# Performance work log

Measured on AMD Instinct MI355X. Metric: run time of the kernel, lower is better.

## Reference

```python
import jax, jax.numpy as jnp
import numpy as np

B, N, C_IN, C_OUT = 2, 512, 64, 64  # mid_dim == out_dim
EPS = 1e-5

def _bn(x, g, b):
    # PyTorch BatchNorm1d in training mode: biased batch stats over axis 0 of [M, C]
    mu = x.mean(axis=0)
    var = x.var(axis=0)
    return (x - mu) * jax.lax.rsqrt(var + EPS) * g + b

def setup_inputs() -> dict:
    key = jax.random.key(0)
    ks = jax.random.split(key, 16)
    s = 0.05
    return {
        "pos": jax.random.normal(ks[0], (B, N, 3), jnp.float32),
        "c_features": jax.random.normal(ks[1], (B, N, C_IN), jnp.float32),
        "Wq": jax.random.normal(ks[2], (C_OUT, C_IN), jnp.float32) * s,
        "bq": jnp.zeros((C_OUT,), jnp.float32),
        "Wk": jax.random.normal(ks[3], (C_OUT, C_IN), jnp.float32) * s,
        "bk": jnp.zeros((C_OUT,), jnp.float32),
        "Wv": jax.random.normal(ks[4], (C_OUT, C_IN), jnp.float32) * s,
        "bv": jnp.zeros((C_OUT,), jnp.float32),
        "Wp1": jax.random.normal(ks[5], (3, 3), jnp.float32) * s,
        "bp1": jnp.zeros((3,), jnp.float32),
        "g_p": jnp.ones((3,), jnp.float32),
        "b_p": jnp.zeros((3,), jnp.float32),
        "Wp2": jax.random.normal(ks[6], (C_OUT, 3), jnp.float32) * s,
        "bp2": jnp.zeros((C_OUT,), jnp.float32),
        "g_w": jnp.ones((C_OUT,), jnp.float32),
        "b_w": jnp.zeros((C_OUT,), jnp.float32),
        "Ww1": jax.random.normal(ks[7], (C_OUT, C_OUT), jnp.float32) * s,
        "bw1": jnp.zeros((C_OUT,), jnp.float32),
        "Ww2": jax.random.normal(ks[8], (C_OUT, C_OUT), jnp.float32) * s,
        "bw2": jnp.zeros((C_OUT,), jnp.float32),
    }

def reference(pos, c_features, Wq, bq, Wk, bk, Wv, bv, Wp1, bp1, g_p, b_p, Wp2, bp2, g_w, b_w, Ww1, bw1, Ww2, bw2):
    b, n = pos.shape[0], pos.shape[1]
    q = c_features @ Wq.T + bq                       # [B,N,Cmid]
    k = c_features @ Wk.T + bk
    v = c_features @ Wv.T + bv                       # [B,N,Cout]
    rel = pos[:, :, None, :] - pos[:, None, :, :]    # [B,N,N,3]
    h = rel.reshape(-1, 3) @ Wp1.T + bp1             # [B*N*N,3]
    h = jax.nn.relu(_bn(h, g_p, b_p))
    delta = (h @ Wp2.T + bp2).reshape(b, n, n, -1)   # [B,N,N,Cmid]
    qk = q[:, :, None, :] - k[:, None, :, :] + delta # [B,N,N,Cmid]
    h2 = _bn(qk.reshape(-1, qk.shape[-1]), g_w, b_w)
    h2 = jax.nn.relu(h2)
    h2 = jax.nn.relu(h2 @ Ww1.T + bw1)
    w = (h2 @ Ww2.T + bw2).reshape(b, n, n, -1)      # [B,N,N,Cout]
    attn = jax.nn.softmax(w, axis=2)                 # softmax over j
    out = jnp.sum(attn * (v[:, None, :, :] + delta), axis=2)  # [B,N,Cout]
    return out
```

## Files before the change

kernel.cpp:

```cpp
#include <hip/hip_runtime.h>
#include <stdint.h>
#include <stddef.h>

#define DEV __device__ __forceinline__

typedef __attribute__((ext_vector_type(4))) float f32x4;
typedef __attribute__((ext_vector_type(8))) short bf16x8;

union FragU { bf16x8 f; uint32_t u[4]; };

DEV uint32_t pk_bf16(float a, float b) {
  uint32_t d;
  asm("v_cvt_pk_bf16_f32 %0, %1, %2" : "=v"(d) : "v"(a), "v"(b));
  return d;
}

DEV uint16_t f2bf(float x) {
  uint32_t u = __float_as_uint(x);
  u += 0x7fffu + ((u >> 16) & 1u);
  return (uint16_t)(u >> 16);
}

__launch_bounds__(256)
__global__ void kAll(const float* __restrict__ cf, const float* __restrict__ pos,
                     const float* __restrict__ Wq, const float* __restrict__ Wk,
                     const float* __restrict__ Wv, const float* __restrict__ bq,
                     const float* __restrict__ bk, const float* __restrict__ bv,
                     const float* __restrict__ Ww1, const float* __restrict__ Ww2,
                     const float* __restrict__ Wp1, const float* __restrict__ g_p,
                     const float* __restrict__ b_p, const float* __restrict__ bp2,
                     float* __restrict__ qo, float* __restrict__ ko,
                     float* __restrict__ vT, uint16_t* __restrict__ W1bf,
                     uint16_t* __restrict__ W2bf, float* __restrict__ hpa,
                     float* __restrict__ Mpart, float* __restrict__ XPp,
                     float* __restrict__ SNp) {
  const int bid = blockIdx.x, t = threadIdx.x;

  __shared__ __align__(16) float Ush[4160];
  __shared__ __align__(16) f32x4 X[512];
  __shared__ float redr[64][4][4];
  __shared__ float mred[256][6];
  __shared__ float mred2[64][6];
  __shared__ float rfin[64][4];
  __shared__ float redn[256][2];
  __shared__ float wred[4][2][9];
  __shared__ float a1L[3];

  if (bid < 128) {
    const int c = t & 63, rr = t >> 6;
    const int r0 = bid * 8;
    float accq[2], acck[2], accv[2];
    for (int m = 0; m < 3; ++m) {
      __syncthreads();
      const float* Wm = (m == 0) ? Wq : ((m == 1) ? Wk : Wv);
      for (int idx = t; idx < 4096; idx += 256)
        Ush[(idx & 63) * 65 + (idx >> 6)] = Wm[idx];
      __syncthreads();
#pragma unroll
      for (int rp = 0; rp < 2; ++rp) {
        const int row = r0 + rr + 4 * rp;
        const float* cfr = cf + (size_t)row * 64;
        float a = 0.f;
#pragma unroll 8
        for (int kk = 0; kk < 64; ++kk)
          a = fmaf(cfr[kk], Ush[kk * 65 + c], a);
        if (m == 0) accq[rp] = a;
        else if (m == 1) acck[rp] = a;
        else accv[rp] = a;
      }
    }
#pragma unroll
    for (int rp = 0; rp < 2; ++rp) {
      const int bn = r0 + rr + 4 * rp;
      qo[(size_t)bn * 64 + c] = accq[rp] + bq[c];
      ko[(size_t)bn * 64 + c] = acck[rp] + bk[c];
    }
    float* vb = (float*)X;
    const float bvv = bv[c] + bp2[c];
    vb[c * 12 + rr] = accv[0] + bvv;
    vb[c * 12 + rr + 4] = accv[1] + bvv;
    __syncthreads();
    if (t < 128) {
      const int c2 = t >> 1, hf = t & 1;
      const f32x4 v = *(const f32x4*)(vb + c2 * 12 + 4 * hf);
      *(f32x4*)(vT + ((size_t)(r0 >> 9) * 64 + c2) * 512 + (r0 & 511) + 4 * hf) = v;
    }
  } else if (bid == 128) {
    const float L2E = 1.4426950408889634f;
    for (int idx = t; idx < 8192; idx += 256) {
      const int m = idx >> 12;
      const int r = idx & 4095;
      const int f = r >> 9;
      const int l = (r >> 3) & 63;
      const int e = r & 7;
      const int nt = f >> 1, ks = f & 1, lm = l & 15, lq = l >> 4;
      const int row = 16 * nt + lm, col = 8 * lq + 32 * ks + e;
      const float src = m ? (Ww2[row * 64 + col] * L2E) : Ww1[row * 64 + col];
      (m ? W2bf : W1bf)[r] = f2bf(src);
    }
  } else {
    const int sb = bid - 129;
    const int s = sb >> 4, b = (sb >> 3) & 1, chunk = sb & 7;
    const int r0g = b * 512 + chunk * 64;

    {
      const int w = t >> 6, c = t & 63;
      const float* wr = (s ? Wk : Wq) + c * 64;
      const float bias = s ? bk[c] : (bq[c] + bp2[c]);
      f32x4 wreg[16];
#pragma unroll
      for (int kv = 0; kv < 16; ++kv) wreg[kv] = *(const f32x4*)(wr + kv * 4);
      for (int m = 0; m < 16; ++m) {
        const int row = w * 16 + m;
        const f32x4* cfr = (const f32x4*)(cf + (size_t)(r0g + row) * 64);
        float a0 = bias, a1v = 0.f, a2v = 0.f, a3v = 0.f;
#pragma unroll
        for (int kv = 0; kv < 16; ++kv) {
          const f32x4 f = cfr[kv];
          a0 = fmaf(f.x, wreg[kv].x, a0);
          a1v = fmaf(f.y, wreg[kv].y, a1v);
          a2v = fmaf(f.z, wreg[kv].z, a2v);
          a3v = fmaf(f.w, wreg[kv].w, a3v);
        }
        Ush[row * 64 + c] = (a0 + a1v) + (a2v + a3v);
      }
    }

    {
      const int l = t & 63, wid = t >> 6;
      for (int b2 = 0; b2 < 2; ++b2) {
        float s9[9] = {0, 0, 0, 0, 0, 0, 0, 0, 0};
        for (int r = 0; r < 2; ++r) {
          const int row = t + 256 * r;
          const float* p = pos + (size_t)(b2 * 512 + row) * 3;
          const float p0 = p[0], p1 = p[1], p2 = p[2];
          s9[0] += p0; s9[1] += p1; s9[2] += p2;
          s9[3] += p0 * p0; s9[4] += p0 * p1; s9[5] += p0 * p2;
          s9[6] += p1 * p1; s9[7] += p1 * p2; s9[8] += p2 * p2;
        }
#pragma unroll
        for (int a = 0; a < 9; ++a) {
          float v = s9[a];
          v += __shfl_xor(v, 1);  v += __shfl_xor(v, 2);  v += __shfl_xor(v, 4);
          v += __shfl_xor(v, 8);  v += __shfl_xor(v, 16); v += __shfl_xor(v, 32);
          s9[a] = v;
        }
        if (l == 0) {
#pragma unroll
          for (int a = 0; a < 9; ++a) wred[wid][b2][a] = s9[a];
        }
      }
    }
    __syncthreads();
    if (t == 0) {
      float C[6] = {0, 0, 0, 0, 0, 0};
      const float invM = 1.0f / 524288.0f;
      for (int b2 = 0; b2 < 2; ++b2) {
        float acc9[9];
#pragma unroll
        for (int a = 0; a < 9; ++a)
          acc9[a] = wred[0][b2][a] + wred[1][b2][a] + wred[2][b2][a] + wred[3][b2][a];
        C[0] += 1024.f * acc9[3] - 2.f * acc9[0] * acc9[0];
        C[1] += 1024.f * acc9[4] - 2.f * acc9[0] * acc9[1];
        C[2] += 1024.f * acc9[5] - 2.f * acc9[0] * acc9[2];
        C[3] += 1024.f * acc9[6] - 2.f * acc9[1] * acc9[1];
        C[4] += 1024.f * acc9[7] - 2.f * acc9[1] * acc9[2];
        C[5] += 1024.f * acc9[8] - 2.f * acc9[2] * acc9[2];
      }
      for (int a = 0; a < 6; ++a) C[a] *= invM;
      for (int tt = 0; tt < 3; ++tt) {
        const float w0 = Wp1[tt * 3 + 0], w1 = Wp1[tt * 3 + 1], w2 = Wp1[tt * 3 + 2];
        const float var = w0 * w0 * C[0] + w1 * w1 * C[3] + w2 * w2 * C[5]
                        + 2.f * (w0 * w1 * C[1] + w0 * w2 * C[2] + w1 * w2 * C[4]);
        a1L[tt] = g_p[tt] * rsqrtf(var + 1e-5f);
      }
    }
    __syncthreads();

    {
      const float a10 = a1L[0], a11 = a1L[1], a12 = a1L[2];
      const float w00 = Wp1[0], w01 = Wp1[1], w02 = Wp1[2];
      const float w10 = Wp1[3], w11 = Wp1[4], w12 = Wp1[5];
      const float w20 = Wp1[6], w21 = Wp1[7], w22 = Wp1[8];
      for (int r = 0; r < 2; ++r) {
        const int row = t + 256 * r;
        const float* p = pos + (size_t)(b * 512 + row) * 3;
        const float p0 = p[0], p1 = p[1], p2 = p[2];
        f32x4 v;
        v.x = a10 * (w00 * p0 + w01 * p1 + w02 * p2);
        v.y = a11 * (w10 * p0 + w11 * p1 + w12 * p2);
        v.z = a12 * (w20 * p0 + w21 * p1 + w22 * p2);
        v.w = 0.f;
        if (s == 0 && chunk == 0)
          *(f32x4*)(hpa + (size_t)(b * 512 + row) * 4) = v;
        if (s) { v.x = -v.x; v.y = -v.y; v.z = -v.z; }
        X[row] = v;
      }
    }
    __syncthreads();

    {
      const int al = t >> 2, qr = t & 3;
      const int a = chunk * 64 + al;
      const f32x4 xa = X[a];
      const float base0 = xa.x + b_p[0], base1 = xa.y + b_p[1], base2 = xa.z + b_p[2];
      float r0 = 0, r1 = 0, r2 = 0;
      float m00 = 0, m01 = 0, m02 = 0, m11 = 0, m12 = 0, m22 = 0;
#pragma unroll 8
      for (int jj = qr * 128; jj < qr * 128 + 128; ++jj) {
        const f32x4 xj = X[jj];
        const float h0 = fmaxf(0.f, base0 - xj.x);
        const float h1 = fmaxf(0.f, base1 - xj.y);
        const float h2 = fmaxf(0.f, base2 - xj.z);
        r0 += h0; r1 += h1; r2 += h2;
        if (s == 0) {
          m00 = fmaf(h0, h0, m00); m01 = fmaf(h0, h1, m01); m02 = fmaf(h0, h2, m02);
          m11 = fmaf(h1, h1, m11); m12 = fmaf(h1, h2, m12); m22 = fmaf(h2, h2, m22);
        }
      }
      redr[al][qr][0] = r0; redr[al][qr][1] = r1; redr[al][qr][2] = r2; redr[al][qr][3] = 0.f;
      mred[t][0] = m00; mred[t][1] = m01; mred[t][2] = m02;
      mred[t][3] = m11; mred[t][4] = m12; mred[t][5] = m22;
    }
    __syncthreads();

    if (t < 64) {
      float sx = 0, sy = 0, sz = 0;
#pragma unroll
      for (int p = 0; p < 4; ++p) { sx += redr[t][p][0]; sy += redr[t][p][1]; sz += redr[t][p][2]; }
      rfin[t][0] = sx; rfin[t][1] = sy; rfin[t][2] = sz; rfin[t][3] = 0.f;
      if (s == 0) {
#pragma unroll
        for (int cc = 0; cc < 6; ++cc)
          mred2[t][cc] = mred[t][cc] + mred[t + 64][cc] + mred[t + 128][cc] + mred[t + 192][cc];
      }
    }
    __syncthreads();

    if (s == 0 && t < 6) {
      float m = 0.f;
      for (int p = 0; p < 64; ++p) m += mred2[p][t];
      Mpart[sb * 12 + t] = m;
    }
    if (s == 0 && t >= 64 && t < 67) {
      const int tt = t - 64;
      float v = 0.f;
#pragma unroll 8
      for (int a = 0; a < 64; ++a) v += rfin[a][tt];
      Mpart[sb * 12 + 6 + tt] = v;
    }
    if (t < 192) {
      const int c = t & 63, tt = t >> 6;
      float xp = 0.f;
#pragma unroll 8
      for (int a = 0; a < 64; ++a) xp = fmaf(Ush[a * 64 + c], rfin[a][tt], xp);
      if (s) xp = -xp;
      XPp[((size_t)sb * 3 + tt) * 64 + c] = xp;
    }
    {
      const int c = t & 63, g = t >> 6;
      float su = 0.f, su2 = 0.f;
#pragma unroll
      for (int r = 0; r < 16; ++r) {
        const float v = Ush[(g * 16 + r) * 64 + c];
        su += v;
        su2 = fmaf(v, v, su2);
      }
      redn[t][0] = su; redn[t][1] = su2;
    }
    __syncthreads();
    if (t < 64) {
      float a0 = 0.f, a1v = 0.f;
#pragma unroll
      for (int p = 0; p < 4; ++p) { a0 += redn[t + 64 * p][0]; a1v += redn[t + 64 * p][1]; }
      SNp[((size_t)sb * 2 + 0) * 64 + t] = a0;
      SNp[((size_t)sb * 2 + 1) * 64 + t] = a1v;
    }
  }
}

__launch_bounds__(256)
__global__ void k3_main(const float* __restrict__ q, const float* __restrict__ kk_,
                        const float* __restrict__ vT, const float* __restrict__ hpa,
                        const float* __restrict__ Mpart, const float* __restrict__ XPp,
                        const float* __restrict__ SNp, const float* __restrict__ g_w,
                        const float* __restrict__ b_w,
                        const uint16_t* __restrict__ W1bf, const uint16_t* __restrict__ W2bf,
                        const float* __restrict__ bp2, const float* __restrict__ Wp2,
                        const float* __restrict__ b_p, const float* __restrict__ bw1g,
                        const float* __restrict__ bw2g, float* __restrict__ out) {
  const int bid = blockIdx.x;
  const int b = bid >> 9, i = bid & 511;
  const int t = threadIdx.x;
  const int wid = t >> 6, l = t & 63;
  const int lm = l & 15, lq = l >> 4;

  __shared__ __align__(16) uint16_t W1l[4096];
  __shared__ __align__(16) uint16_t W2l[4096];
  __shared__ __align__(16) uint16_t H2[4][16][76];
  __shared__ __align__(16) float P0[64];
  __shared__ __align__(16) float a2s[64];
  __shared__ __align__(16) float Pts[3][64];
  __shared__ __align__(16) float comb[4][64][2];
  __shared__ float xps[4][3][64];
  __shared__ float sns[4][2][64];
  __shared__ float msh[12];

  {
    *(bf16x8*)(&W1l[t * 16])     = *(const bf16x8*)(W1bf + t * 16);
    *(bf16x8*)(&W1l[t * 16 + 8]) = *(const bf16x8*)(W1bf + t * 16 + 8);
    *(bf16x8*)(&W2l[t * 16])     = *(const bf16x8*)(W2bf + t * 16);
    *(bf16x8*)(&W2l[t * 16 + 8]) = *(const bf16x8*)(W2bf + t * 16 + 8);
  }

  {
    const int qd = t >> 6, c = t & 63;
    float x0 = 0, x1 = 0, x2 = 0, s0 = 0, s1 = 0;
#pragma unroll
    for (int p = 0; p < 8; ++p) {
      const int blk = qd * 8 + p;
      x0 += XPp[((size_t)blk * 3 + 0) * 64 + c];
      x1 += XPp[((size_t)blk * 3 + 1) * 64 + c];
      x2 += XPp[((size_t)blk * 3 + 2) * 64 + c];
      s0 += SNp[((size_t)blk * 2 + 0) * 64 + c];
      s1 += SNp[((size_t)blk * 2 + 1) * 64 + c];
    }
    xps[qd][0][c] = x0; xps[qd][1][c] = x1; xps[qd][2][c] = x2;
    sns[qd][0][c] = s0; sns[qd][1][c] = s1;
    if (t < 12) {
      float m = 0.f;
#pragma unroll
      for (int p = 0; p < 16; ++p) m += Mpart[p * 12 + t];
      msh[t] = m;
    }
  }
  __syncthreads();

  if (t < 64) {
    const int c = t;
    const float URd0 = xps[0][0][c] + xps[1][0][c] + xps[2][0][c] + xps[3][0][c];
    const float URd1 = xps[0][1][c] + xps[1][1][c] + xps[2][1][c] + xps[3][1][c];
    const float URd2 = xps[0][2][c] + xps[1][2][c] + xps[2][2][c] + xps[3][2][c];
    const float Su0 = sns[0][0][c], Su20 = sns[0][1][c];
    const float Su1 = sns[1][0][c], Su21 = sns[1][1][c];
    const float Sk0 = sns[2][0][c], Sk20 = sns[2][1][c];
    const float Sk1 = sns[3][0][c], Sk21 = sns[3][1][c];
    const float P0t = Wp2[c * 3 + 0], P1t = Wp2[c * 3 + 1], P2t = Wp2[c * 3 + 2];
    const float Nf = 512.f, invM = 1.f / 524288.f;
    float S1 = Nf * (Su0 - Sk0) + Nf * (Su1 - Sk1);
    const float Q2 = Nf * Su20 - 2.f * Su0 * Sk0 + Nf * Sk20
                   + Nf * Su21 - 2.f * Su1 * Sk1 + Nf * Sk21;
    const float Xc = P0t * URd0 + P1t * URd1 + P2t * URd2;
    S1 += P0t * msh[6] + P1t * msh[7] + P2t * msh[8];
    const float Hm = P0t * P0t * msh[0] + 2.f * P0t * P1t * msh[1] + 2.f * P0t * P2t * msh[2]
                   + P1t * P1t * msh[3] + 2.f * P1t * P2t * msh[4] + P2t * P2t * msh[5];
    const float E1 = S1 * invM;
    const float E2 = (Q2 + 2.f * Xc + Hm) * invM;
    const float var = E2 - E1 * E1;
    const float A2 = g_w[c] * rsqrtf(var + 1e-5f);
    const float be2 = b_w[c] - E1 * A2;
    a2s[c] = A2;
    P0[c] = fmaf(A2, q[(size_t)(b * 512 + i) * 64 + c] + bp2[c], be2);
    Pts[0][c] = A2 * P0t;
    Pts[1][c] = A2 * P1t;
    Pts[2][c] = A2 * P2t;
  }

  const f32x4 hi = *(const f32x4*)(hpa + (size_t)(b * 512 + i) * 4);
  const float bb0 = b_p[0], bb1 = b_p[1], bb2 = b_p[2];
  const float LOG2E = 1.4426950408889634f;

  float bw1r[4], bw2l[4], wpa[4], wpb[4], wpc[4];
#pragma unroll
  for (int nt = 0; nt < 4; ++nt) {
    const int c = 16 * nt + lm;
    bw1r[nt] = bw1g[c];
    bw2l[nt] = bw2g[c] * LOG2E;
    wpa[nt] = Wp2[c * 3 + 0];
    wpb[nt] = Wp2[c * 3 + 1];
    wpc[nt] = Wp2[c * 3 + 2];
  }

  float l_[4] = {0.f, 0.f, 0.f, 0.f};
  float acc_[4] = {0.f, 0.f, 0.f, 0.f};

  __syncthreads();

  const float* kbase = kk_ + (size_t)(b * 512) * 64;
  const float* hbase = hpa + (size_t)(b * 512) * 4;
  const float* vTb = vT + (size_t)b * 64 * 512;

  f32x4 kvA[2][2];
  {
    const int j0 = wid * 16 + lm;
#pragma unroll
    for (int ks = 0; ks < 2; ++ks) {
      kvA[ks][0] = *(const f32x4*)(kbase + (size_t)j0 * 64 + 32 * ks + 8 * lq);
      kvA[ks][1] = *(const f32x4*)(kbase + (size_t)j0 * 64 + 32 * ks + 8 * lq + 4);
    }
  }

  for (int it = 0; it < 8; ++it) {
    const int jb = it * 64 + wid * 16;
    const int j = jb + lm;
    const int j2 = jb + 4 * lq;

    f32x4 kvN[2][2];
    if (it < 7) {
      const int jn = j + 64;
#pragma unroll
      for (int ks = 0; ks < 2; ++ks) {
        kvN[ks][0] = *(const f32x4*)(kbase + (size_t)jn * 64 + 32 * ks + 8 * lq);
        kvN[ks][1] = *(const f32x4*)(kbase + (size_t)jn * 64 + 32 * ks + 8 * lq + 4);
      }
    }

    const f32x4 hj = *(const f32x4*)(hbase + j * 4);
    f32x4 hjr[4];
#pragma unroll
    for (int r = 0; r < 4; ++r) hjr[r] = *(const f32x4*)(hbase + (j2 + r) * 4);
    f32x4 vv[4];
#pragma unroll
    for (int nt = 0; nt < 4; ++nt)
      vv[nt] = *(const f32x4*)(vTb + (size_t)(16 * nt + lm) * 512 + j2);

    const float h0 = fmaxf(0.f, hi.x - hj.x + bb0);
    const float h1 = fmaxf(0.f, hi.y - hj.y + bb1);
    const float h2v = fmaxf(0.f, hi.z - hj.z + bb2);

    FragU A1[2];
#pragma unroll
    for (int ks = 0; ks < 2; ++ks) {
      const int c0 = 32 * ks + 8 * lq;
      f32x4 pv[2], av[2], t0[2], t1[2], t2[2];
      pv[0] = *(const f32x4*)(P0 + c0);        pv[1] = *(const f32x4*)(P0 + c0 + 4);
      av[0] = *(const f32x4*)(a2s + c0);       av[1] = *(const f32x4*)(a2s + c0 + 4);
      t0[0] = *(const f32x4*)(&Pts[0][c0]);    t0[1] = *(const f32x4*)(&Pts[0][c0 + 4]);
      t1[0] = *(const f32x4*)(&Pts[1][c0]);    t1[1] = *(const f32x4*)(&Pts[1][c0 + 4]);
      t2[0] = *(const f32x4*)(&Pts[2][c0]);    t2[1] = *(const f32x4*)(&Pts[2][c0 + 4]);
      float x[8];
#pragma unroll
      for (int e = 0; e < 8; ++e) {
        const int hh = e >> 2, e4 = e & 3;
        float xv = pv[hh][e4] - av[hh][e4] * kvA[ks][hh][e4];
        xv = fmaf(t0[hh][e4], h0, xv);
        xv = fmaf(t1[hh][e4], h1, xv);
        xv = fmaf(t2[hh][e4], h2v, xv);
        x[e] = fmaxf(0.f, xv);
      }
      A1[ks].u[0] = pk_bf16(x[0], x[1]);
      A1[ks].u[1] = pk_bf16(x[2], x[3]);
      A1[ks].u[2] = pk_bf16(x[4], x[5]);
      A1[ks].u[3] = pk_bf16(x[6], x[7]);
    }

    f32x4 d1[4];
    __builtin_amdgcn_s_setprio(1);
#pragma unroll
    for (int nt = 0; nt < 4; ++nt) {
      FragU b0, b1;
      b0.f = *(const bf16x8*)(&W1l[((nt * 2 + 0) * 64 + l) * 8]);
      b1.f = *(const bf16x8*)(&W1l[((nt * 2 + 1) * 64 + l) * 8]);
      f32x4 z = {bw1r[nt], bw1r[nt], bw1r[nt], bw1r[nt]};
      z = __builtin_amdgcn_mfma_f32_16x16x32_bf16(A1[0].f, b0.f, z, 0, 0, 0);
      z = __builtin_amdgcn_mfma_f32_16x16x32_bf16(A1[1].f, b1.f, z, 0, 0, 0);
      d1[nt] = z;
    }
    __builtin_amdgcn_s_setprio(0);

    uint16_t (*h2w)[76] = H2[wid];
#pragma unroll
    for (int nt = 0; nt < 4; ++nt) {
      const uint32_t u01 = pk_bf16(fmaxf(0.f, d1[nt][0]), fmaxf(0.f, d1[nt][1]));
      const uint32_t u23 = pk_bf16(fmaxf(0.f, d1[nt][2]), fmaxf(0.f, d1[nt][3]));
      const int col = 16 * nt + lm;
      h2w[4 * lq + 0][col] = (uint16_t)(u01 & 0xffffu);
      h2w[4 * lq + 1][col] = (uint16_t)(u01 >> 16);
      h2w[4 * lq + 2][col] = (uint16_t)(u23 & 0xffffu);
      h2w[4 * lq + 3][col] = (uint16_t)(u23 >> 16);
    }

    FragU A2[2];
    A2[0].f = *(const bf16x8*)(&h2w[lm][8 * lq]);
    A2[1].f = *(const bf16x8*)(&h2w[lm][32 + 8 * lq]);

    f32x4 d2[4];
    __builtin_amdgcn_s_setprio(1);
#pragma unroll
    for (int nt = 0; nt < 4; ++nt) {
      FragU b0, b1;
      b0.f = *(const bf16x8*)(&W2l[((nt * 2 + 0) * 64 + l) * 8]);
      b1.f = *(const bf16x8*)(&W2l[((nt * 2 + 1) * 64 + l) * 8]);
      f32x4 z = {bw2l[nt], bw2l[nt], bw2l[nt], bw2l[nt]};
      z = __builtin_amdgcn_mfma_f32_16x16x32_bf16(A2[0].f, b0.f, z, 0, 0, 0);
      z = __builtin_amdgcn_mfma_f32_16x16x32_bf16(A2[1].f, b1.f, z, 0, 0, 0);
      d2[nt] = z;
    }
    __builtin_amdgcn_s_setprio(0);

    float hr0[4], hr1[4], hr2[4];
#pragma unroll
    for (int r = 0; r < 4; ++r) {
      hr0[r] = fmaxf(0.f, hi.x - hjr[r].x + bb0);
      hr1[r] = fmaxf(0.f, hi.y - hjr[r].y + bb1);
      hr2[r] = fmaxf(0.f, hi.z - hjr[r].z + bb2);
    }

#pragma unroll
    for (int nt = 0; nt < 4; ++nt) {
      float p[4], val[4];
#pragma unroll
      for (int r = 0; r < 4; ++r) {
        p[r] = __builtin_amdgcn_exp2f(d2[nt][r]);
        float v0 = vv[nt][r];
        v0 = fmaf(wpa[nt], hr0[r], v0);
        v0 = fmaf(wpb[nt], hr1[r], v0);
        v0 = fmaf(wpc[nt], hr2[r], v0);
        val[r] = v0;
      }
      l_[nt] += (p[0] + p[1]) + (p[2] + p[3]);
      float a = acc_[nt];
      a = fmaf(p[0], val[0], a);
      a = fmaf(p[1], val[1], a);
      a = fmaf(p[2], val[2], a);
      a = fmaf(p[3], val[3], a);
      acc_[nt] = a;
    }

    if (it < 7) {
#pragma unroll
      for (int ks = 0; ks < 2; ++ks) {
        kvA[ks][0] = kvN[ks][0];
        kvA[ks][1] = kvN[ks][1];
      }
    }
  }

#pragma unroll
  for (int nt = 0; nt < 4; ++nt) {
    l_[nt] += __shfl_xor(l_[nt], 16);
    acc_[nt] += __shfl_xor(acc_[nt], 16);
    l_[nt] += __shfl_xor(l_[nt], 32);
    acc_[nt] += __shfl_xor(acc_[nt], 32);
  }
  if (lq == 0) {
#pragma unroll
    for (int nt = 0; nt < 4; ++nt) {
      comb[wid][16 * nt + lm][0] = l_[nt];
      comb[wid][16 * nt + lm][1] = acc_[nt];
    }
  }
  __syncthreads();
  if (t < 64) {
    float L = 0.f, A = 0.f;
#pragma unroll
    for (int w = 0; w < 4; ++w) {
      L += comb[w][t][0];
      A += comb[w][t][1];
    }
    out[(size_t)(b * 512 + i) * 64 + t] = A / L;
  }
}

extern "C" void kernel_launch(void* const* d_in, const int* in_sizes, int n_in,
                              void* d_out, int out_size, void* d_ws, size_t ws_size,
                              hipStream_t stream) {
  (void)in_sizes; (void)n_in; (void)out_size; (void)ws_size;
  const float* pos = (const float*)d_in[0];
  const float* cf  = (const float*)d_in[1];
  const float* Wq  = (const float*)d_in[2];
  const float* bq  = (const float*)d_in[3];
  const float* Wk  = (const float*)d_in[4];
  const float* bk  = (const float*)d_in[5];
  const float* Wv  = (const float*)d_in[6];
  const float* bv  = (const float*)d_in[7];
  const float* Wp1 = (const float*)d_in[8];
  const float* g_p = (const float*)d_in[10];
  const float* b_p = (const float*)d_in[11];
  const float* Wp2 = (const float*)d_in[12];
  const float* bp2 = (const float*)d_in[13];
  const float* g_w = (const float*)d_in[14];
  const float* b_w = (const float*)d_in[15];
  const float* Ww1 = (const float*)d_in[16];
  const float* bw1 = (const float*)d_in[17];
  const float* Ww2 = (const float*)d_in[18];
  const float* bw2 = (const float*)d_in[19];

  char* ws = (char*)d_ws;
  uint16_t* W1bf = (uint16_t*)(ws + 0);
  uint16_t* W2bf = (uint16_t*)(ws + 8192);
  float*    hpaw = (float*)(ws + 16896);
  float*    qw   = (float*)(ws + 33280);
  float*    kw   = (float*)(ws + 295424);
  float*    vTw  = (float*)(ws + 557568);
  float*    Mpw  = (float*)(ws + 821248);
  float*    XPpw = (float*)(ws + 823040);
  float*    SNpw = (float*)(ws + 847872);

  kAll<<<dim3(161), dim3(256), 0, stream>>>(cf, pos, Wq, Wk, Wv, bq, bk, bv,
                                            Ww1, Ww2, Wp1, g_p, b_p, bp2,
                                            qw, kw, vTw, W1bf, W2bf, hpaw,
                                            Mpw, XPpw, SNpw);
  k3_main<<<dim3(1024), dim3(256), 0, stream>>>(qw, kw, vTw, hpaw, Mpw, XPpw, SNpw,
                                                g_w, b_w, W1bf, W2bf, bp2, Wp2, b_p,
                                                bw1, bw2, (float*)d_out);
}
```

Baseline: 69.97 us.

## Switch attention MLP to fp16 with packed half2 prologue math and fp16 keys

Replaces the bf16 MFMA path with f16 MFMAs and converts the weight prepacking to fp16. The per-pair BN/affine/ReLU prologue now runs as packed half2 FMAs on fp16 per-channel constants, instead of scalar fp32 math followed by bf16 packing. Keys are stored in fp16, which halves their global load traffic. The s_setprio hints are dropped. The aim is to cut VALU work and memory traffic in the inner loop, at the cost of reduced precision and range in the prologue arithmetic.

```diff
diff --git a/kernel.cpp b/kernel.cpp
--- a/kernel.cpp
+++ b/kernel.cpp
@@ -1,25 +1,18 @@
 #include <hip/hip_runtime.h>
+#include <hip/hip_fp16.h>
 #include <stdint.h>
 #include <stddef.h>
 
 #define DEV __device__ __forceinline__
 
 typedef __attribute__((ext_vector_type(4))) float f32x4;
-typedef __attribute__((ext_vector_type(8))) short bf16x8;
-
-union FragU { bf16x8 f; uint32_t u[4]; };
-
-DEV uint32_t pk_bf16(float a, float b) {
-  uint32_t d;
-  asm("v_cvt_pk_bf16_f32 %0, %1, %2" : "=v"(d) : "v"(a), "v"(b));
-  return d;
-}
-
-DEV uint16_t f2bf(float x) {
-  uint32_t u = __float_as_uint(x);
-  u += 0x7fffu + ((u >> 16) & 1u);
-  return (uint16_t)(u >> 16);
-}
+typedef __attribute__((ext_vector_type(8))) _Float16 f16x8;
+typedef __attribute__((ext_vector_type(2))) _Float16 h2;
+
+union FragH { f16x8 f; uint32_t u[4]; h2 h[4]; };
+union V4H { f32x4 v; h2 h[4]; };
+
+DEV uint16_t f2h(float x) { return __half_as_ushort(__float2half_rn(x)); }
 
 __launch_bounds__(256)
 __global__ void kAll(const float* __restrict__ cf, const float* __restrict__ pos,
@@ -29,9 +22,9 @@
                      const float* __restrict__ Ww1, const float* __restrict__ Ww2,
                      const float* __restrict__ Wp1, const float* __restrict__ g_p,
                      const float* __restrict__ b_p, const float* __restrict__ bp2,
-                     float* __restrict__ qo, float* __restrict__ ko,
-                     float* __restrict__ vT, uint16_t* __restrict__ W1bf,
-                     uint16_t* __restrict__ W2bf, float* __restrict__ hpa,
+                     float* __restrict__ qo, uint16_t* __restrict__ kh,
+                     float* __restrict__ vT, uint16_t* __restrict__ W1h,
+                     uint16_t* __restrict__ W2h, float* __restrict__ hpa,
                      float* __restrict__ Mpart, float* __restrict__ XPp,
                      float* __restrict__ SNp) {
   const int bid = blockIdx.x, t = threadIdx.x;
@@ -73,7 +66,7 @@
     for (int rp = 0; rp < 2; ++rp) {
       const int bn = r0 + rr + 4 * rp;
       qo[(size_t)bn * 64 + c] = accq[rp] + bq[c];
-      ko[(size_t)bn * 64 + c] = acck[rp] + bk[c];
+      kh[(size_t)bn * 64 + c] = f2h(acck[rp] + bk[c]);
     }
     float* vb = (float*)X;
     const float bvv = bv[c] + bp2[c];
@@ -96,7 +89,7 @@
       const int nt = f >> 1, ks = f & 1, lm = l & 15, lq = l >> 4;
       const int row = 16 * nt + lm, col = 8 * lq + 32 * ks + e;
       const float src = m ? (Ww2[row * 64 + col] * L2E) : Ww1[row * 64 + col];
-      (m ? W2bf : W1bf)[r] = f2bf(src);
+      (m ? W2h : W1h)[r] = f2h(src);
     }
   } else {
     const int sb = bid - 129;
@@ -211,11 +204,11 @@
         const f32x4 xj = X[jj];
         const float h0 = fmaxf(0.f, base0 - xj.x);
         const float h1 = fmaxf(0.f, base1 - xj.y);
-        const float h2 = fmaxf(0.f, base2 - xj.z);
-        r0 += h0; r1 += h1; r2 += h2;
+        const float h2v = fmaxf(0.f, base2 - xj.z);
+        r0 += h0; r1 += h1; r2 += h2v;
         if (s == 0) {
-          m00 = fmaf(h0, h0, m00); m01 = fmaf(h0, h1, m01); m02 = fmaf(h0, h2, m02);
-          m11 = fmaf(h1, h1, m11); m12 = fmaf(h1, h2, m12); m22 = fmaf(h2, h2, m22);
+          m00 = fmaf(h0, h0, m00); m01 = fmaf(h0, h1, m01); m02 = fmaf(h0, h2v, m02);
+          m11 = fmaf(h1, h1, m11); m12 = fmaf(h1, h2v, m12); m22 = fmaf(h2v, h2v, m22);
         }
       }
       redr[al][qr][0] = r0; redr[al][qr][1] = r1; redr[al][qr][2] = r2; redr[al][qr][3] = 0.f;
@@ -280,7 +273,7 @@
 }
 
 __launch_bounds__(256)
-__global__ void k3_main(const float* __restrict__ q, const float* __restrict__ kk_,
+__global__ void k3_main(const float* __restrict__ q, const uint16_t* __restrict__ kh,
                         const float* __restrict__ vT, const float* __restrict__ hpa,
                         const float* __restrict__ Mpart, const float* __restrict__ XPp,
                         const float* __restrict__ SNp, const float* __restrict__ g_w,
@@ -298,19 +291,21 @@
   __shared__ __align__(16) uint16_t W1l[4096];
   __shared__ __align__(16) uint16_t W2l[4096];
   __shared__ __align__(16) uint16_t H2[4][16][76];
-  __shared__ __align__(16) float P0[64];
-  __shared__ __align__(16) float a2s[64];
-  __shared__ __align__(16) float Pts[3][64];
+  __shared__ __align__(16) uint16_t P0h[64];
+  __shared__ __align__(16) uint16_t nA2h[64];
+  __shared__ __align__(16) uint16_t Pt0h[64];
+  __shared__ __align__(16) uint16_t Pt1h[64];
+  __shared__ __align__(16) uint16_t Pt2h[64];
   __shared__ __align__(16) float comb[4][64][2];
   __shared__ float xps[4][3][64];
   __shared__ float sns[4][2][64];
   __shared__ float msh[12];
 
   {
-    *(bf16x8*)(&W1l[t * 16])     = *(const bf16x8*)(W1bf + t * 16);
-    *(bf16x8*)(&W1l[t * 16 + 8]) = *(const bf16x8*)(W1bf + t * 16 + 8);
-    *(bf16x8*)(&W2l[t * 16])     = *(const bf16x8*)(W2bf + t * 16);
-    *(bf16x8*)(&W2l[t * 16 + 8]) = *(const bf16x8*)(W2bf + t * 16 + 8);
+    *(f16x8*)(&W1l[t * 16])     = *(const f16x8*)(W1bf + t * 16);
+    *(f16x8*)(&W1l[t * 16 + 8]) = *(const f16x8*)(W1bf + t * 16 + 8);
+    *(f16x8*)(&W2l[t * 16])     = *(const f16x8*)(W2bf + t * 16);
+    *(f16x8*)(&W2l[t * 16 + 8]) = *(const f16x8*)(W2bf + t * 16 + 8);
   }
 
   {
@@ -359,11 +354,11 @@
     const float var = E2 - E1 * E1;
     const float A2 = g_w[c] * rsqrtf(var + 1e-5f);
     const float be2 = b_w[c] - E1 * A2;
-    a2s[c] = A2;
-    P0[c] = fmaf(A2, q[(size_t)(b * 512 + i) * 64 + c] + bp2[c], be2);
-    Pts[0][c] = A2 * P0t;
-    Pts[1][c] = A2 * P1t;
-    Pts[2][c] = A2 * P2t;
+    P0h[c] = f2h(fmaf(A2, q[(size_t)(b * 512 + i) * 64 + c] + bp2[c], be2));
+    nA2h[c] = f2h(-A2);
+    Pt0h[c] = f2h(A2 * P0t);
+    Pt1h[c] = f2h(A2 * P1t);
+    Pt2h[c] = f2h(A2 * P2t);
   }
 
   const f32x4 hi = *(const f32x4*)(hpa + (size_t)(b * 512 + i) * 4);
@@ -386,18 +381,16 @@
 
   __syncthreads();
 
-  const float* kbase = kk_ + (size_t)(b * 512) * 64;
+  const uint16_t* kbase = kh + (size_t)(b * 512) * 64;
   const float* hbase = hpa + (size_t)(b * 512) * 4;
   const float* vTb = vT + (size_t)b * 64 * 512;
 
-  f32x4 kvA[2][2];
+  f32x4 kvA[2];
   {
     const int j0 = wid * 16 + lm;
 #pragma unroll
-    for (int ks = 0; ks < 2; ++ks) {
-      kvA[ks][0] = *(const f32x4*)(kbase + (size_t)j0 * 64 + 32 * ks + 8 * lq);
-      kvA[ks][1] = *(const f32x4*)(kbase + (size_t)j0 * 64 + 32 * ks + 8 * lq + 4);
-    }
+    for (int ks = 0; ks < 2; ++ks)
+      kvA[ks] = *(const f32x4*)(kbase + (size_t)j0 * 64 + 32 * ks + 8 * lq);
   }
 
   for (int it = 0; it < 8; ++it) {
@@ -405,14 +398,12 @@
     const int j = jb + lm;
     const int j2 = jb + 4 * lq;
 
-    f32x4 kvN[2][2];
+    f32x4 kvN[2];
     if (it < 7) {
       const int jn = j + 64;
 #pragma unroll
-      for (int ks = 0; ks < 2; ++ks) {
-        kvN[ks][0] = *(const f32x4*)(kbase + (size_t)jn * 64 + 32 * ks + 8 * lq);
-        kvN[ks][1] = *(const f32x4*)(kbase + (size_t)jn * 64 + 32 * ks + 8 * lq + 4);
-      }
+      for (int ks = 0; ks < 2; ++ks)
+        kvN[ks] = *(const f32x4*)(kbase + (size_t)jn * 64 + 32 * ks + 8 * lq);
     }
 
     const f32x4 hj = *(const f32x4*)(hbase + j * 4);
@@ -427,76 +418,70 @@
     const float h0 = fmaxf(0.f, hi.x - hj.x + bb0);
     const float h1 = fmaxf(0.f, hi.y - hj.y + bb1);
     const float h2v = fmaxf(0.f, hi.z - hj.z + bb2);
-
-    FragU A1[2];
+    const _Float16 h0s = (_Float16)h0, h1s = (_Float16)h1, h2s = (_Float16)h2v;
+    const h2 h0h = {h0s, h0s};
+    const h2 h1h = {h1s, h1s};
+    const h2 h2h = {h2s, h2s};
+    const h2 z2 = {(_Float16)0.f, (_Float16)0.f};
+
+    FragH A1[2];
 #pragma unroll
     for (int ks = 0; ks < 2; ++ks) {
       const int c0 = 32 * ks + 8 * lq;
-      f32x4 pv[2], av[2], t0[2], t1[2], t2[2];
-      pv[0] = *(const f32x4*)(P0 + c0);        pv[1] = *(const f32x4*)(P0 + c0 + 4);
-      av[0] = *(const f32x4*)(a2s + c0);       av[1] = *(const f32x4*)(a2s + c0 + 4);
-      t0[0] = *(const f32x4*)(&Pts[0][c0]);    t0[1] = *(const f32x4*)(&Pts[0][c0 + 4]);
-      t1[0] = *(const f32x4*)(&Pts[1][c0]);    t1[1] = *(const f32x4*)(&Pts[1][c0 + 4]);
-      t2[0] = *(const f32x4*)(&Pts[2][c0]);    t2[1] = *(const f32x4*)(&Pts[2][c0 + 4]);
-      float x[8];
-#pragma unroll
-      for (int e = 0; e < 8; ++e) {
-        const int hh = e >> 2, e4 = e & 3;
-        float xv = pv[hh][e4] - av[hh][e4] * kvA[ks][hh][e4];
-        xv = fmaf(t0[hh][e4], h0, xv);
-        xv = fmaf(t1[hh][e4], h1, xv);
-        xv = fmaf(t2[hh][e4], h2v, xv);
-        x[e] = fmaxf(0.f, xv);
-      }
-      A1[ks].u[0] = pk_bf16(x[0], x[1]);
-      A1[ks].u[1] = pk_bf16(x[2], x[3]);
-      A1[ks].u[2] = pk_bf16(x[4], x[5]);
-      A1[ks].u[3] = pk_bf16(x[6], x[7]);
+      V4H pv, na, t0, t1, t2, kv;
+      pv.v = *(const f32x4*)(P0h + c0);
+      na.v = *(const f32x4*)(nA2h + c0);
+      t0.v = *(const f32x4*)(Pt0h + c0);
+      t1.v = *(const f32x4*)(Pt1h + c0);
+      t2.v = *(const f32x4*)(Pt2h + c0);
+      kv.v = kvA[ks];
+#pragma unroll
+      for (int e = 0; e < 4; ++e) {
+        h2 xv = na.h[e] * kv.h[e] + pv.h[e];
+        xv = t0.h[e] * h0h + xv;
+        xv = t1.h[e] * h1h + xv;
+        xv = t2.h[e] * h2h + xv;
+        A1[ks].h[e] = __builtin_elementwise_max(xv, z2);
+      }
     }
 
     f32x4 d1[4];
-    __builtin_amdgcn_s_setprio(1);
 #pragma unroll
     for (int nt = 0; nt < 4; ++nt) {
-      FragU b0, b1;
-      b0.f = *(const bf16x8*)(&W1l[((nt * 2 + 0) * 64 + l) * 8]);
-      b1.f = *(const bf16x8*)(&W1l[((nt * 2 + 1) * 64 + l) * 8]);
+      FragH b0, b1;
+      b0.f = *(const f16x8*)(&W1l[((nt * 2 + 0) * 64 + l) * 8]);
+      b1.f = *(const f16x8*)(&W1l[((nt * 2 + 1) * 64 + l) * 8]);
       f32x4 z = {bw1r[nt], bw1r[nt], bw1r[nt], bw1r[nt]};
-      z = __builtin_amdgcn_mfma_f32_16x16x32_bf16(A1[0].f, b0.f, z, 0, 0, 0);
-      z = __builtin_amdgcn_mfma_f32_16x16x32_bf16(A1[1].f, b1.f, z, 0, 0, 0);
+      z = __builtin_amdgcn_mfma_f32_16x16x32_f16(A1[0].f, b0.f, z, 0, 0, 0);
+      z = __builtin_amdgcn_mfma_f32_16x16x32_f16(A1[1].f, b1.f, z, 0, 0, 0);
       d1[nt] = z;
     }
-    __builtin_amdgcn_s_setprio(0);
 
     uint16_t (*h2w)[76] = H2[wid];
 #pragma unroll
     for (int nt = 0; nt < 4; ++nt) {
-      const uint32_t u01 = pk_bf16(fmaxf(0.f, d1[nt][0]), fmaxf(0.f, d1[nt][1]));
-      const uint32_t u23 = pk_bf16(fmaxf(0.f, d1[nt][2]), fmaxf(0.f, d1[nt][3]));
       const int col = 16 * nt + lm;
-      h2w[4 * lq + 0][col] = (uint16_t)(u01 & 0xffffu);
-      h2w[4 * lq + 1][col] = (uint16_t)(u01 >> 16);
-      h2w[4 * lq + 2][col] = (uint16_t)(u23 & 0xffffu);
-      h2w[4 * lq + 3][col] = (uint16_t)(u23 >> 16);
-    }
-
-    FragU A2[2];
-    A2[0].f = *(const bf16x8*)(&h2w[lm][8 * lq]);
-    A2[1].f = *(const bf16x8*)(&h2w[lm][32 + 8 * lq]);
+      h2w[4 * lq + 0][col] = f2h(fmaxf(0.f, d1[nt][0]));
+      h2w[4 * lq + 1][col] = f2h(fmaxf(0.f, d1[nt][1]));
+      h2w[4 * lq + 2][col] = f2h(fmaxf(0.f, d1[nt][2]));
+      h2w[4 * lq + 3][col] = f2h(fmaxf(0.f, d1[nt][3]));
+    }
+
+    FragH A2[2];
+    A2[0].f = *(const f16x8*)(&h2w[lm][8 * lq]);
+    A2[1].f = *(const f16x8*)(&h2w[lm][32 + 8 * lq]);
 
     f32x4 d2[4];
-    __builtin_amdgcn_s_setprio(1);
 #pragma unroll
     for (int nt = 0; nt < 4; ++nt) {
-      FragU b0, b1;
-      b0.f = *(const bf16x8*)(&W2l[((nt * 2 + 0) * 64 + l) * 8]);
-      b1.f = *(const bf16x8*)(&W2l[((nt * 2 + 1) * 64 + l) * 8]);
+      FragH b0, b1;
+      b0.f = *(const f16x8*)(&W2l[((nt * 2 + 0) * 64 + l) * 8]);
+      b1.f = *(const f16x8*)(&W2l[((nt * 2 + 1) * 64 + l) * 8]);
       f32x4 z = {bw2l[nt], bw2l[nt], bw2l[nt], bw2l[nt]};
-      z = __builtin_amdgcn_mfma_f32_16x16x32_bf16(A2[0].f, b0.f, z, 0, 0, 0);
-      z = __builtin_amdgcn_mfma_f32_16x16x32_bf16(A2[1].f, b1.f, z, 0, 0, 0);
+      z = __builtin_amdgcn_mfma_f32_16x16x32_f16(A2[0].f, b0.f, z, 0, 0, 0);
+      z = __builtin_amdgcn_mfma_f32_16x16x32_f16(A2[1].f, b1.f, z, 0, 0, 0);
       d2[nt] = z;
     }
-    __builtin_amdgcn_s_setprio(0);
 
     float hr0[4], hr1[4], hr2[4];
 #pragma unroll
@@ -528,11 +513,8 @@
     }
 
     if (it < 7) {
-#pragma unroll
-      for (int ks = 0; ks < 2; ++ks) {
-        kvA[ks][0] = kvN[ks][0];
-        kvA[ks][1] = kvN[ks][1];
-      }
+      kvA[0] = kvN[0];
+      kvA[1] = kvN[1];
     }
   }
 
@@ -587,11 +569,11 @@
   const float* bw2 = (const float*)d_in[19];
 
   char* ws = (char*)d_ws;
-  uint16_t* W1bf = (uint16_t*)(ws + 0);
-  uint16_t* W2bf = (uint16_t*)(ws + 8192);
+  uint16_t* W1h  = (uint16_t*)(ws + 0);
+  uint16_t* W2h  = (uint16_t*)(ws + 8192);
   float*    hpaw = (float*)(ws + 16896);
   float*    qw   = (float*)(ws + 33280);
-  float*    kw   = (float*)(ws + 295424);
+  uint16_t* khw  = (uint16_t*)(ws + 295424);
   float*    vTw  = (float*)(ws + 557568);
   float*    Mpw  = (float*)(ws + 821248);
   float*    XPpw = (float*)(ws + 823040);
@@ -599,9 +581,9 @@
 
   kAll<<<dim3(161), dim3(256), 0, stream>>>(cf, pos, Wq, Wk, Wv, bq, bk, bv,
                                             Ww1, Ww2, Wp1, g_p, b_p, bp2,
-                                            qw, kw, vTw, W1bf, W2bf, hpaw,
+                                            qw, khw, vTw, W1h, W2h, hpaw,
                                             Mpw, XPpw, SNpw);
-  k3_main<<<dim3(1024), dim3(256), 0, stream>>>(qw, kw, vTw, hpaw, Mpw, XPpw, SNpw,
-                                                g_w, b_w, W1bf, W2bf, bp2, Wp2, b_p,
+  k3_main<<<dim3(1024), dim3(256), 0, stream>>>(qw, khw, vTw, hpaw, Mpw, XPpw, SNpw,
+                                                g_w, b_w, W1h, W2h, bp2, Wp2, b_p,
                                                 bw1, bw2, (float*)d_out);
 }
```

Result: slower. 73.73 us (+5.4%).

## Finalize BN statistics once in last kAll block instead of per k3 block

Applied to the files above, without the earlier changes.

The BatchNorm2 statistics (scale, shift, scaled Wp2 rows) were previously reduced from partial sums in every one of the 1024 k3_main blocks. This computation moves into the last-finishing stats block of kAll, using an atomic counter plus threadfence, and writes the final per-channel values to workspace for k3_main to read directly. This removes redundant global reads, reductions and a barrier from each k3 block. The price is an extra memset launch and a serial tail in one kAll block. It also removes the s_setprio hints around the MFMA loops.

```diff
diff --git a/kernel.cpp b/kernel.cpp
--- a/kernel.cpp
+++ b/kernel.cpp
@@ -29,11 +29,15 @@
                      const float* __restrict__ Ww1, const float* __restrict__ Ww2,
                      const float* __restrict__ Wp1, const float* __restrict__ g_p,
                      const float* __restrict__ b_p, const float* __restrict__ bp2,
+                     const float* __restrict__ g_w, const float* __restrict__ b_w,
+                     const float* __restrict__ Wp2,
                      float* __restrict__ qo, float* __restrict__ ko,
                      float* __restrict__ vT, uint16_t* __restrict__ W1bf,
                      uint16_t* __restrict__ W2bf, float* __restrict__ hpa,
                      float* __restrict__ Mpart, float* __restrict__ XPp,
-                     float* __restrict__ SNp) {
+                     float* __restrict__ SNp, unsigned int* __restrict__ counter,
+                     float* __restrict__ a2o, float* __restrict__ be2o,
+                     float* __restrict__ PtT) {
   const int bid = blockIdx.x, t = threadIdx.x;
 
   __shared__ __align__(16) float Ush[4160];
@@ -45,6 +49,9 @@
   __shared__ float redn[256][2];
   __shared__ float wred[4][2][9];
   __shared__ float a1L[3];
+  __shared__ float MfS[6];
+  __shared__ float ShfS[3];
+  __shared__ unsigned int isLast;
 
   if (bid < 128) {
     const int c = t & 63, rr = t >> 6;
@@ -211,11 +218,11 @@
         const f32x4 xj = X[jj];
         const float h0 = fmaxf(0.f, base0 - xj.x);
         const float h1 = fmaxf(0.f, base1 - xj.y);
-        const float h2 = fmaxf(0.f, base2 - xj.z);
-        r0 += h0; r1 += h1; r2 += h2;
+        const float h2v = fmaxf(0.f, base2 - xj.z);
+        r0 += h0; r1 += h1; r2 += h2v;
         if (s == 0) {
-          m00 = fmaf(h0, h0, m00); m01 = fmaf(h0, h1, m01); m02 = fmaf(h0, h2, m02);
-          m11 = fmaf(h1, h1, m11); m12 = fmaf(h1, h2, m12); m22 = fmaf(h2, h2, m22);
+          m00 = fmaf(h0, h0, m00); m01 = fmaf(h0, h1, m01); m02 = fmaf(h0, h2v, m02);
+          m11 = fmaf(h1, h1, m11); m12 = fmaf(h1, h2v, m12); m22 = fmaf(h2v, h2v, m22);
         }
       }
       redr[al][qr][0] = r0; redr[al][qr][1] = r1; redr[al][qr][2] = r2; redr[al][qr][3] = 0.f;
@@ -276,15 +283,86 @@
       SNp[((size_t)sb * 2 + 0) * 64 + t] = a0;
       SNp[((size_t)sb * 2 + 1) * 64 + t] = a1v;
     }
+
+    __syncthreads();
+    if (t == 0) {
+      __threadfence();
+      const unsigned int old = atomicAdd(counter, 1u);
+      isLast = (old == 31u) ? 1u : 0u;
+    }
+    __syncthreads();
+    if (isLast) {
+      __threadfence();
+      if (t < 6) {
+        float m = 0.f;
+#pragma unroll
+        for (int p = 0; p < 16; ++p) m += Mpart[p * 12 + t];
+        MfS[t] = m;
+      }
+      if (t >= 6 && t < 9) {
+        const int tt = t - 6;
+        float v = 0.f;
+#pragma unroll
+        for (int p = 0; p < 16; ++p) v += Mpart[p * 12 + 6 + tt];
+        ShfS[tt] = v;
+      }
+      __syncthreads();
+      if (t < 64) {
+        const int c = t;
+        float Su[2], Su2[2], Sk[2], Sk2[2];
+#pragma unroll
+        for (int bb = 0; bb < 2; ++bb) {
+          float a0 = 0.f, a1v = 0.f, a2v = 0.f, a3 = 0.f;
+#pragma unroll
+          for (int p = 0; p < 8; ++p) {
+            const int blkU = bb * 8 + p;
+            const int blkK = 16 + bb * 8 + p;
+            a0 += SNp[((size_t)blkU * 2 + 0) * 64 + c];
+            a1v += SNp[((size_t)blkU * 2 + 1) * 64 + c];
+            a2v += SNp[((size_t)blkK * 2 + 0) * 64 + c];
+            a3 += SNp[((size_t)blkK * 2 + 1) * 64 + c];
+          }
+          Su[bb] = a0; Su2[bb] = a1v; Sk[bb] = a2v; Sk2[bb] = a3;
+        }
+        float URd0 = 0.f, URd1 = 0.f, URd2 = 0.f;
+#pragma unroll
+        for (int blk = 0; blk < 32; ++blk) {
+          URd0 += XPp[((size_t)blk * 3 + 0) * 64 + c];
+          URd1 += XPp[((size_t)blk * 3 + 1) * 64 + c];
+          URd2 += XPp[((size_t)blk * 3 + 2) * 64 + c];
+        }
+        const float P0t = Wp2[c * 3 + 0], P1t = Wp2[c * 3 + 1], P2t = Wp2[c * 3 + 2];
+        const float Nf = 512.f, invM = 1.f / 524288.f;
+        float S1 = 0.f, Q2 = 0.f;
+#pragma unroll
+        for (int bb = 0; bb < 2; ++bb) {
+          S1 += Nf * (Su[bb] - Sk[bb]);
+          Q2 += Nf * Su2[bb] - 2.f * Su[bb] * Sk[bb] + Nf * Sk2[bb];
+        }
+        const float Xc = P0t * URd0 + P1t * URd1 + P2t * URd2;
+        S1 += P0t * ShfS[0] + P1t * ShfS[1] + P2t * ShfS[2];
+        const float Hm = P0t * P0t * MfS[0] + 2.f * P0t * P1t * MfS[1] + 2.f * P0t * P2t * MfS[2]
+                       + P1t * P1t * MfS[3] + 2.f * P1t * P2t * MfS[4] + P2t * P2t * MfS[5];
+        const float E1 = S1 * invM;
+        const float E2 = (Q2 + 2.f * Xc + Hm) * invM;
+        const float var = E2 - E1 * E1;
+        const float rstd = rsqrtf(var + 1e-5f);
+        const float A2 = g_w[c] * rstd;
+        a2o[c] = A2;
+        be2o[c] = b_w[c] - E1 * A2;
+        PtT[0 * 64 + c] = A2 * P0t;
+        PtT[1 * 64 + c] = A2 * P1t;
+        PtT[2 * 64 + c] = A2 * P2t;
+      }
+    }
   }
 }
 
 __launch_bounds__(256)
 __global__ void k3_main(const float* __restrict__ q, const float* __restrict__ kk_,
                         const float* __restrict__ vT, const float* __restrict__ hpa,
-                        const float* __restrict__ Mpart, const float* __restrict__ XPp,
-                        const float* __restrict__ SNp, const float* __restrict__ g_w,
-                        const float* __restrict__ b_w,
+                        const float* __restrict__ a2g, const float* __restrict__ be2g,
+                        const float* __restrict__ PtTg,
                         const uint16_t* __restrict__ W1bf, const uint16_t* __restrict__ W2bf,
                         const float* __restrict__ bp2, const float* __restrict__ Wp2,
                         const float* __restrict__ b_p, const float* __restrict__ bw1g,
@@ -302,9 +380,6 @@
   __shared__ __align__(16) float a2s[64];
   __shared__ __align__(16) float Pts[3][64];
   __shared__ __align__(16) float comb[4][64][2];
-  __shared__ float xps[4][3][64];
-  __shared__ float sns[4][2][64];
-  __shared__ float msh[12];
 
   {
     *(bf16x8*)(&W1l[t * 16])     = *(const bf16x8*)(W1bf + t * 16);
@@ -312,58 +387,13 @@
     *(bf16x8*)(&W2l[t * 16])     = *(const bf16x8*)(W2bf + t * 16);
     *(bf16x8*)(&W2l[t * 16 + 8]) = *(const bf16x8*)(W2bf + t * 16 + 8);
   }
-
-  {
-    const int qd = t >> 6, c = t & 63;
-    float x0 = 0, x1 = 0, x2 = 0, s0 = 0, s1 = 0;
-#pragma unroll
-    for (int p = 0; p < 8; ++p) {
-      const int blk = qd * 8 + p;
-      x0 += XPp[((size_t)blk * 3 + 0) * 64 + c];
-      x1 += XPp[((size_t)blk * 3 + 1) * 64 + c];
-      x2 += XPp[((size_t)blk * 3 + 2) * 64 + c];
-      s0 += SNp[((size_t)blk * 2 + 0) * 64 + c];
-      s1 += SNp[((size_t)blk * 2 + 1) * 64 + c];
-    }
-    xps[qd][0][c] = x0; xps[qd][1][c] = x1; xps[qd][2][c] = x2;
-    sns[qd][0][c] = s0; sns[qd][1][c] = s1;
-    if (t < 12) {
-      float m = 0.f;
-#pragma unroll
-      for (int p = 0; p < 16; ++p) m += Mpart[p * 12 + t];
-      msh[t] = m;
-    }
-  }
-  __syncthreads();
-
   if (t < 64) {
-    const int c = t;
-    const float URd0 = xps[0][0][c] + xps[1][0][c] + xps[2][0][c] + xps[3][0][c];
-    const float URd1 = xps[0][1][c] + xps[1][1][c] + xps[2][1][c] + xps[3][1][c];
-    const float URd2 = xps[0][2][c] + xps[1][2][c] + xps[2][2][c] + xps[3][2][c];
-    const float Su0 = sns[0][0][c], Su20 = sns[0][1][c];
-    const float Su1 = sns[1][0][c], Su21 = sns[1][1][c];
-    const float Sk0 = sns[2][0][c], Sk20 = sns[2][1][c];
-    const float Sk1 = sns[3][0][c], Sk21 = sns[3][1][c];
-    const float P0t = Wp2[c * 3 + 0], P1t = Wp2[c * 3 + 1], P2t = Wp2[c * 3 + 2];
-    const float Nf = 512.f, invM = 1.f / 524288.f;
-    float S1 = Nf * (Su0 - Sk0) + Nf * (Su1 - Sk1);
-    const float Q2 = Nf * Su20 - 2.f * Su0 * Sk0 + Nf * Sk20
-                   + Nf * Su21 - 2.f * Su1 * Sk1 + Nf * Sk21;
-    const float Xc = P0t * URd0 + P1t * URd1 + P2t * URd2;
-    S1 += P0t * msh[6] + P1t * msh[7] + P2t * msh[8];
-    const float Hm = P0t * P0t * msh[0] + 2.f * P0t * P1t * msh[1] + 2.f * P0t * P2t * msh[2]
-                   + P1t * P1t * msh[3] + 2.f * P1t * P2t * msh[4] + P2t * P2t * msh[5];
-    const float E1 = S1 * invM;
-    const float E2 = (Q2 + 2.f * Xc + Hm) * invM;
-    const float var = E2 - E1 * E1;
-    const float A2 = g_w[c] * rsqrtf(var + 1e-5f);
-    const float be2 = b_w[c] - E1 * A2;
-    a2s[c] = A2;
-    P0[c] = fmaf(A2, q[(size_t)(b * 512 + i) * 64 + c] + bp2[c], be2);
-    Pts[0][c] = A2 * P0t;
-    Pts[1][c] = A2 * P1t;
-    Pts[2][c] = A2 * P2t;
+    const float a2v = a2g[t];
+    a2s[t] = a2v;
+    P0[t] = fmaf(a2v, q[(size_t)(b * 512 + i) * 64 + t] + bp2[t], be2g[t]);
+  } else {
+    const int idx = t - 64;
+    if (idx < 192) Pts[idx >> 6][idx & 63] = PtTg[idx];
   }
 
   const f32x4 hi = *(const f32x4*)(hpa + (size_t)(b * 512 + i) * 4);
@@ -455,7 +485,6 @@
     }
 
     f32x4 d1[4];
-    __builtin_amdgcn_s_setprio(1);
 #pragma unroll
     for (int nt = 0; nt < 4; ++nt) {
       FragU b0, b1;
@@ -466,7 +495,6 @@
       z = __builtin_amdgcn_mfma_f32_16x16x32_bf16(A1[1].f, b1.f, z, 0, 0, 0);
       d1[nt] = z;
     }
-    __builtin_amdgcn_s_setprio(0);
 
     uint16_t (*h2w)[76] = H2[wid];
 #pragma unroll
@@ -485,7 +513,6 @@
     A2[1].f = *(const bf16x8*)(&h2w[lm][32 + 8 * lq]);
 
     f32x4 d2[4];
-    __builtin_amdgcn_s_setprio(1);
 #pragma unroll
     for (int nt = 0; nt < 4; ++nt) {
       FragU b0, b1;
@@ -496,7 +523,6 @@
       z = __builtin_amdgcn_mfma_f32_16x16x32_bf16(A2[1].f, b1.f, z, 0, 0, 0);
       d2[nt] = z;
     }
-    __builtin_amdgcn_s_setprio(0);
 
     float hr0[4], hr1[4], hr2[4];
 #pragma unroll
@@ -587,21 +613,28 @@
   const float* bw2 = (const float*)d_in[19];
 
   char* ws = (char*)d_ws;
-  uint16_t* W1bf = (uint16_t*)(ws + 0);
-  uint16_t* W2bf = (uint16_t*)(ws + 8192);
-  float*    hpaw = (float*)(ws + 16896);
-  float*    qw   = (float*)(ws + 33280);
-  float*    kw   = (float*)(ws + 295424);
-  float*    vTw  = (float*)(ws + 557568);
-  float*    Mpw  = (float*)(ws + 821248);
-  float*    XPpw = (float*)(ws + 823040);
-  float*    SNpw = (float*)(ws + 847872);
-
+  uint16_t*     W1bf = (uint16_t*)(ws + 0);
+  uint16_t*     W2bf = (uint16_t*)(ws + 8192);
+  unsigned int* cnt  = (unsigned int*)(ws + 16384);
+  float*        hpaw = (float*)(ws + 16896);
+  float*        qw   = (float*)(ws + 33280);
+  float*        kw   = (float*)(ws + 295424);
+  float*        vTw  = (float*)(ws + 557568);
+  float*        a2w  = (float*)(ws + 819712);
+  float*        be2w = (float*)(ws + 819968);
+  float*        PtTw = (float*)(ws + 820224);
+  float*        Mpw  = (float*)(ws + 821248);
+  float*        XPpw = (float*)(ws + 823040);
+  float*        SNpw = (float*)(ws + 847872);
+
+  hipMemsetAsync(cnt, 0, sizeof(unsigned int), stream);
   kAll<<<dim3(161), dim3(256), 0, stream>>>(cf, pos, Wq, Wk, Wv, bq, bk, bv,
                                             Ww1, Ww2, Wp1, g_p, b_p, bp2,
+                                            g_w, b_w, Wp2,
                                             qw, kw, vTw, W1bf, W2bf, hpaw,
-                                            Mpw, XPpw, SNpw);
-  k3_main<<<dim3(1024), dim3(256), 0, stream>>>(qw, kw, vTw, hpaw, Mpw, XPpw, SNpw,
-                                                g_w, b_w, W1bf, W2bf, bp2, Wp2, b_p,
-                                                bw1, bw2, (float*)d_out);
+                                            Mpw, XPpw, SNpw, cnt,
+                                            a2w, be2w, PtTw);
+  k3_main<<<dim3(1024), dim3(256), 0, stream>>>(qw, kw, vTw, hpaw, a2w, be2w, PtTw,
+                                                W1bf, W2bf, bp2, Wp2, b_p, bw1, bw2,
+                                                (float*)d_out);
 }
```

Result: slower. 74.63 us (+6.7%).
